# Optimization experiments

Measured on AMD Instinct MI355X. Metric: run time of the kernel, lower is better.

## Reference

```python
import jax, jax.numpy as jnp
import numpy as np

B, L, S, H, E, M = 16, 2048, 2048, 8, 64, 64  # batch, q len, kv len, heads, per-head dim, modes
SCALE = 1.0 / (512 * 512)  # 1/(in_channels*out_channels)


def setup_inputs() -> dict:
    key = jax.random.key(0)
    kq, kk, kv, kw1, kw2 = jax.random.split(key, 5)
    return {
        "q": jax.random.normal(kq, (B, L, H, E), dtype=jnp.float32),
        "k": jax.random.normal(kk, (B, S, H, E), dtype=jnp.float32),
        "v": jax.random.normal(kv, (B, S, H, E), dtype=jnp.float32),
        "weights_real": SCALE * jax.random.uniform(kw1, (H, E, E, M), dtype=jnp.float32),
        "weights_imag": SCALE * jax.random.uniform(kw2, (H, E, E, M), dtype=jnp.float32),
        "mask": jnp.zeros((1,), dtype=bool),  # unused by forward (kept for signature parity)
    }


def reference(q, k, v, weights_real, weights_imag, mask):
    # [B, L, H, E] -> [B, H, E, L]
    _q = jnp.transpose(q, (0, 2, 3, 1))
    _k = jnp.transpose(k, (0, 2, 3, 1))
    _v = jnp.transpose(v, (0, 2, 3, 1))

    # rFFT along time; mode_select_method='else' => index = range(M), a contiguous slice
    Qf = jnp.fft.rfft(_q, axis=-1)[..., :M]  # [B, H, E, M] complex
    Kf = jnp.fft.rfft(_k, axis=-1)[..., :M]
    Vf = jnp.fft.rfft(_v, axis=-1)[..., :M]

    # cross attention in frequency domain
    QK = jnp.einsum('bhex,bhey->bhxy', Qf, Kf)  # [B, H, M, M] complex
    QK = jnp.tanh(QK.real) + 1j * jnp.tanh(QK.imag)  # 'tanh' activation on re/im
    QKV = jnp.einsum('bhxy,bhey->bhex', QK, Vf)  # [B, H, E, M]

    W = (weights_real + 1j * weights_imag).astype(jnp.complex64)  # [H, E, O, M]
    QKVW = jnp.einsum('bhex,heox->bhox', QKV, W)  # [B, H, O, M]

    # scatter selected modes back into full half-spectrum, then inverse FFT
    Y = jnp.zeros((B, H, E, L // 2 + 1), dtype=jnp.complex64).at[..., :M].set(QKVW)
    y = jnp.fft.irfft(Y, n=L, axis=-1)  # [B, H, O, L] real
    return jnp.transpose(y, (0, 3, 1, 2))  # [B, L, H, O]
```

## Files before the change

### kernel.cpp

```cpp
#include <hip/hip_runtime.h>
#include <hip/hip_fp16.h>
#include <math.h>


#define NB 16
#define NL 2048
#define NH 8
#define NE 64
#define NM 64
#define NHE 512

typedef unsigned short ushort_t;
typedef __attribute__((ext_vector_type(8))) short short8;
typedef __attribute__((ext_vector_type(8))) _Float16 half8;
typedef __attribute__((ext_vector_type(4))) float f32x4;

__device__ inline void gld_lds16(const void* g, void* l) {
    __builtin_amdgcn_global_load_lds((const __attribute__((address_space(1))) unsigned int*)g,
                                     (__attribute__((address_space(3))) unsigned int*)l, 16, 0, 0);
}

__global__ __launch_bounds__(256) void k_tables_gemm(ushort_t* __restrict__ Twh,
                                                     ushort_t* __restrict__ Twl) {
    int i = blockIdx.x * 256 + threadIdx.x;
    int kj = i & 7;
    int l  = (i >> 3) & 63;
    int g  = (i >> 9) & 7;
    int ks = i >> 12;
    int mp = g * 16 + (l & 15);
    int kk = (l >> 4) * 8 + kj;
    int t = ks * 32 + kk;
    int m = mp >> 1;
    float ang = (float)((6.283185307179586476925287 / (double)NL) * (double)((m * t) & (NL - 1)));
    float val = (mp & 1) ? -sinf(ang) : cosf(ang);
    unsigned cb = __float_as_uint(val);
    ushort_t h = (ushort_t)(cb >> 16);
    float lo = val - __uint_as_float(cb & 0xffff0000u);
    unsigned lb = __float_as_uint(lo);
    unsigned r = lb + 0x7fffu + ((lb >> 16) & 1u);
    Twh[i] = h;
    Twl[i] = (ushort_t)(r >> 16);
}

__global__ __launch_bounds__(256) void k_tables_idft(ushort_t* __restrict__ Ih) {
    int i = blockIdx.x * 256 + threadIdx.x;
    int j = i & 7;
    int l = (i >> 3) & 63;
    int f = (i >> 9) & 15;
    int ks = (i >> 13) & 3;
    int tt = i >> 15;
    int t = tt * 256 + f * 16 + (l & 15);
    int kk = ks * 32 + (l >> 4) * 8 + j;
    int x = kk >> 1;
    float ang = (float)((6.283185307179586476925287 / (double)NL) * (double)((t * x) & (NL - 1)));
    float val = (kk & 1) ? -sinf(ang) : cosf(ang);
    Ih[i] = __half_as_ushort(__float2half(val));
}

__global__ __launch_bounds__(256, 3) void k_gemm(
    const float* __restrict__ q, const float* __restrict__ k, const float* __restrict__ v,
    const ushort_t* __restrict__ Twh, const ushort_t* __restrict__ Twl,
    float* __restrict__ Part) {
    const int bx = blockIdx.x & 3;
    const int kq = blockIdx.x >> 2;
    const int b  = blockIdx.y;
    const int z  = blockIdx.z;
    const float* __restrict__ in = (z == 0) ? q : ((z == 1) ? k : v);

    const int tid  = threadIdx.x;
    const int wid  = tid >> 6;
    const int lane = tid & 63;
    const int lr   = lane & 15;
    const int lg   = lane >> 4;

    __shared__ ushort_t Bh[2][4096];
    __shared__ ushort_t Bl[2][4096];

    f32x4 acc[2][8];
#pragma unroll
    for (int f = 0; f < 2; ++f)
#pragma unroll
        for (int g = 0; g < 8; ++g) acc[f][g] = (f32x4){0.f, 0.f, 0.f, 0.f};

    const float* pA = in + ((size_t)b * NL + (size_t)kq * 1024) * NHE + bx * 128 + wid * 32 + lr;

    float arE[2][8], arO[2][8];

#define STAGE_B(n, ksn)                                                               \
    {                                                                                 \
        const ushort_t* gh = Twh + (size_t)(kq * 32 + (ksn)) * 4096;                  \
        const ushort_t* gl = Twl + (size_t)(kq * 32 + (ksn)) * 4096;                  \
        gld_lds16(gh + (size_t)tid * 8, &Bh[n][tid * 8]);                             \
        gld_lds16(gh + (size_t)(tid + 256) * 8, &Bh[n][(tid + 256) * 8]);             \
        gld_lds16(gl + (size_t)tid * 8, &Bl[n][tid * 8]);                             \
        gld_lds16(gl + (size_t)(tid + 256) * 8, &Bl[n][(tid + 256) * 8]);             \
    }

#define LOADA(ar, ksn)                                                                \
    {                                                                                 \
        _Pragma("unroll")                                                             \
        for (int f = 0; f < 2; ++f) {                                                 \
            _Pragma("unroll")                                                         \
            for (int j = 0; j < 8; ++j)                                               \
                ar[f][j] = pA[(size_t)((ksn) * 32 + lg * 8 + j) * NHE + f * 16];      \
        }                                                                             \
    }

#define COMPUTE(ar, n)                                                                \
    {                                                                                 \
        short8 ah[2], al[2];                                                          \
        _Pragma("unroll")                                                             \
        for (int f = 0; f < 2; ++f) {                                                 \
            union { unsigned u[4]; short8 s; } uh, ul;                                \
            _Pragma("unroll")                                                         \
            for (int p = 0; p < 4; ++p) {                                             \
                unsigned b0 = __float_as_uint(ar[f][2 * p]);                          \
                unsigned b1 = __float_as_uint(ar[f][2 * p + 1]);                      \
                uh.u[p] = (b0 >> 16) | (b1 & 0xffff0000u);                            \
                float l0 = ar[f][2 * p]     - __uint_as_float(b0 & 0xffff0000u);      \
                float l1 = ar[f][2 * p + 1] - __uint_as_float(b1 & 0xffff0000u);      \
                unsigned lw;                                                          \
                asm("v_cvt_pk_bf16_f32 %0, %1, %2" : "=v"(lw) : "v"(l0), "v"(l1));    \
                ul.u[p] = lw;                                                         \
            }                                                                         \
            ah[f] = uh.s; al[f] = ul.s;                                               \
        }                                                                             \
        _Pragma("unroll")                                                             \
        for (int g = 0; g < 8; ++g) {                                                 \
            short8 bh8 = *(const short8*)&Bh[n][(g * 64 + lane) * 8];                 \
            short8 bl8 = *(const short8*)&Bl[n][(g * 64 + lane) * 8];                 \
            _Pragma("unroll")                                                         \
            for (int f = 0; f < 2; ++f) {                                             \
                acc[f][g] = __builtin_amdgcn_mfma_f32_16x16x32_bf16(ah[f], bh8, acc[f][g], 0, 0, 0); \
                acc[f][g] = __builtin_amdgcn_mfma_f32_16x16x32_bf16(al[f], bh8, acc[f][g], 0, 0, 0); \
                acc[f][g] = __builtin_amdgcn_mfma_f32_16x16x32_bf16(ah[f], bl8, acc[f][g], 0, 0, 0); \
            }                                                                         \
        }                                                                             \
    }

    STAGE_B(0, 0);
    LOADA(arE, 0);

#pragma unroll 1
    for (int k2 = 0; k2 < 16; ++k2) {
        const int ksB = 2 * k2 + 1;
        __syncthreads();
        STAGE_B(1, ksB);
        LOADA(arO, ksB);
        COMPUTE(arE, 0);
        __syncthreads();
        if (k2 < 15) {
            STAGE_B(0, ksB + 1);
            LOADA(arE, ksB + 1);
        }
        COMPUTE(arO, 1);
    }
#undef STAGE_B
#undef LOADA
#undef COMPUTE

    float* pout = Part + (size_t)(z * 2 + kq) * 1048576;
#pragma unroll
    for (int f = 0; f < 2; ++f) {
#pragma unroll
        for (int g = 0; g < 8; ++g) {
            const int col = g * 16 + lr;
#pragma unroll
            for (int r = 0; r < 4; ++r) {
                const int he = bx * 128 + wid * 32 + f * 16 + 4 * lg + r;
                pout[((size_t)b * NHE + he) * 128 + col] = acc[f][g][r];
            }
        }
    }
}

__global__ __launch_bounds__(256) void k_reduce(
    const float4* __restrict__ Part, float4* __restrict__ Qf,
    float4* __restrict__ Kf, float4* __restrict__ Vf) {
    int i = blockIdx.x * 256 + threadIdx.x;
    int z = i >> 18;
    int r = i & 262143;
    float4 a = Part[(size_t)(z * 2 + 0) * 262144 + r];
    float4 b = Part[(size_t)(z * 2 + 1) * 262144 + r];
    float4 s = make_float4(a.x + b.x, a.y + b.y, a.z + b.z, a.w + b.w);
    float4* o = (z == 0) ? Qf : ((z == 1) ? Kf : Vf);
    o[r] = s;
}

__global__ __launch_bounds__(256) void k_qk(
    const float2* __restrict__ Qf, const float2* __restrict__ Kf,
    float2* __restrict__ QKt) {
    const int bh = blockIdx.x;
    const int xh = blockIdx.y;
    const int tid = threadIdx.x;
    __shared__ float2 Qs[64 * 34];
    __shared__ float2 Ks[64 * 66];

    const float2* Qbase = Qf + (size_t)bh * (NE * NM);
    const float2* Kbase = Kf + (size_t)bh * (NE * NM);
#pragma unroll
    for (int j = 0; j < 4; ++j) {
        int n = tid + j * 256;
        int e = n >> 4, c = n & 15;
        float4 val = ((const float4*)(Qbase + e * NM + xh * 32))[c];
        *((float4*)&Qs[e * 34 + c * 2]) = val;
    }
#pragma unroll
    for (int j = 0; j < 8; ++j) {
        int n = tid + j * 256;
        int e = n >> 5, c = n & 31;
        float4 val = ((const float4*)(Kbase + e * NM))[c];
        *((float4*)&Ks[e * 66 + c * 2]) = val;
    }
    __syncthreads();

    const int yq = tid & 31, xq = tid >> 5;
    float accr[4][2], acci[4][2];
#pragma unroll
    for (int i = 0; i < 4; ++i)
#pragma unroll
        for (int j = 0; j < 2; ++j) { accr[i][j] = 0.f; acci[i][j] = 0.f; }

    for (int e = 0; e < 64; ++e) {
        float4 qa = *((float4*)&Qs[e * 34 + xq * 4]);
        float4 qb = *((float4*)&Qs[e * 34 + xq * 4 + 2]);
        float4 kk = *((float4*)&Ks[e * 66 + yq * 2]);
        float qr[4] = {qa.x, qa.z, qb.x, qb.z};
        float qi[4] = {qa.y, qa.w, qb.y, qb.w};
        float kr[2] = {kk.x, kk.z};
        float ki[2] = {kk.y, kk.w};
#pragma unroll
        for (int i = 0; i < 4; ++i) {
#pragma unroll
            for (int j = 0; j < 2; ++j) {
                accr[i][j] += qr[i] * kr[j] - qi[i] * ki[j];
                acci[i][j] += qr[i] * ki[j] + qi[i] * kr[j];
            }
        }
    }
    const int x0 = xh * 32 + xq * 4;
#pragma unroll
    for (int i = 0; i < 4; ++i) {
        float4 sv = make_float4(tanhf(accr[i][0]), tanhf(acci[i][0]),
                                tanhf(accr[i][1]), tanhf(acci[i][1]));
        *((float4*)&QKt[(size_t)bh * 4096 + (x0 + i) * 64 + yq * 2]) = sv;
    }
}

__global__ __launch_bounds__(256) void k_qkv(
    const float2* __restrict__ Vf, const float2* __restrict__ QKt,
    float2* __restrict__ QKV) {
    const int bh = blockIdx.x;
    const int eh = blockIdx.y;
    const int tid = threadIdx.x;
    __shared__ float2 Vs[32 * 66];
    __shared__ float2 Ps[64 * 66];

    const float2* Vbase = Vf + (size_t)bh * (NE * NM) + eh * 32 * NM;
    const float2* Pbase = QKt + (size_t)bh * 4096;
#pragma unroll
    for (int j = 0; j < 4; ++j) {
        int n = tid + j * 256;
        int r = n >> 5, c = n & 31;
        float4 val = ((const float4*)(Vbase + r * NM))[c];
        *((float4*)&Vs[r * 66 + c * 2]) = val;
    }
#pragma unroll
    for (int j = 0; j < 8; ++j) {
        int n = tid + j * 256;
        int r = n >> 5, c = n & 31;
        float4 val = ((const float4*)(Pbase + r * NM))[c];
        *((float4*)&Ps[r * 66 + c * 2]) = val;
    }
    __syncthreads();

    const int xq = tid & 15, eq2 = tid >> 4;
    const int x0 = xq * 4, e0 = eq2 * 2;
    float accr[2][4], acci[2][4];
#pragma unroll
    for (int i = 0; i < 2; ++i)
#pragma unroll
        for (int j = 0; j < 4; ++j) { accr[i][j] = 0.f; acci[i][j] = 0.f; }

    for (int yy = 0; yy < 64; ++yy) {
        float2 v0 = Vs[(e0 + 0) * 66 + yy];
        float2 v1 = Vs[(e0 + 1) * 66 + yy];
        float2 p0 = Ps[(x0 + 0) * 66 + yy];
        float2 p1 = Ps[(x0 + 1) * 66 + yy];
        float2 p2 = Ps[(x0 + 2) * 66 + yy];
        float2 p3 = Ps[(x0 + 3) * 66 + yy];
        float pr[4] = {p0.x, p1.x, p2.x, p3.x};
        float pi[4] = {p0.y, p1.y, p2.y, p3.y};
#pragma unroll
        for (int j = 0; j < 4; ++j) {
            accr[0][j] += v0.x * pr[j] - v0.y * pi[j];
            acci[0][j] += v0.x * pi[j] + v0.y * pr[j];
            accr[1][j] += v1.x * pr[j] - v1.y * pi[j];
            acci[1][j] += v1.x * pi[j] + v1.y * pr[j];
        }
    }
#pragma unroll
    for (int e = 0; e < 2; ++e) {
        float2* obase = QKV + (size_t)bh * 4096 + (eh * 32 + e0 + e) * 64 + x0;
        float4 s0 = make_float4(accr[e][0], acci[e][0], accr[e][1], acci[e][1]);
        float4 s1 = make_float4(accr[e][2], acci[e][2], accr[e][3], acci[e][3]);
        ((float4*)obase)[0] = s0;
        ((float4*)obase)[1] = s1;
    }
}

__global__ __launch_bounds__(256) void k_wt(
    const float* __restrict__ wr, const float* __restrict__ wi,
    float2* __restrict__ Wt) {
    const int e = blockIdx.x, h = blockIdx.y;
    const int tid = threadIdx.x;
    __shared__ float lr[64 * 68];
    __shared__ float li[64 * 68];
    const float* rbase = wr + (size_t)(h * NE + e) * NE * NM;
    const float* ibase = wi + (size_t)(h * NE + e) * NE * NM;
#pragma unroll
    for (int j = 0; j < 4; ++j) {
        int n = tid + j * 256;
        int o = n >> 4, x4 = n & 15;
        float4 r4 = ((const float4*)(rbase + o * NM))[x4];
        float4 i4 = ((const float4*)(ibase + o * NM))[x4];
        *((float4*)&lr[o * 68 + x4 * 4]) = r4;
        *((float4*)&li[o * 68 + x4 * 4]) = i4;
    }
    __syncthreads();
#pragma unroll
    for (int j = 0; j < 16; ++j) {
        int n = tid + j * 256;
        int x = n >> 6, o = n & 63;
        Wt[((size_t)(h * NM + x) * NE + e) * NE + o] =
            make_float2(lr[o * 68 + x], li[o * 68 + x]);
    }
}

__global__ __launch_bounds__(256) void k_qkvw(
    const float2* __restrict__ QKV, const float2* __restrict__ Wt,
    float2* __restrict__ QKVWs) {
    const int x = blockIdx.x, h = blockIdx.y;
    const int tid = threadIdx.x;
    const int o = tid & 63, bq = tid >> 6;
    float accr[4], acci[4];
#pragma unroll
    for (int j = 0; j < 4; ++j) { accr[j] = 0.f; acci[j] = 0.f; }

    const float2* wbase = Wt + (size_t)(h * NM + x) * NE * NE + o;
    for (int e = 0; e < 64; ++e) {
        float2 w = wbase[(size_t)e * NE];
#pragma unroll
        for (int j = 0; j < 4; ++j) {
            int b = bq * 4 + j;
            float2 a = QKV[((size_t)(b * NH + h) * NE + e) * NM + x];
            accr[j] += a.x * w.x - a.y * w.y;
            acci[j] += a.x * w.y + a.y * w.x;
        }
    }
    const float sc = (x == 0) ? 0.5f : 1.0f;
#pragma unroll
    for (int j = 0; j < 4; ++j) {
        int b = bq * 4 + j;
        QKVWs[((size_t)(b * NH + h) * NM + x) * NE + o] =
            make_float2(accr[j] * sc, acci[j] * sc);
    }
}

__global__ __launch_bounds__(256, 3) void k_idft(
    const float2* __restrict__ QKVWs, const ushort_t* __restrict__ Ih,
    float* __restrict__ yout) {
    const int tt = blockIdx.x;
    const int bh = blockIdx.y;
    const int b = bh >> 3, h = bh & 7;
    const int tid = threadIdx.x;
    const int wid = tid >> 6;
    const int lane = tid & 63;
    const int lr = lane & 15;
    const int lg = lane >> 4;

    __shared__ ushort_t Ta[8192];
    __shared__ unsigned Xs[4096];

    const float2* xb = QKVWs + (size_t)bh * 4096;
#pragma unroll
    for (int r = 0; r < 16; ++r) {
        int i = tid + r * 256;
        int x = i >> 6, o = i & 63;
        float2 val = xb[i];
        int ks = x >> 4;
        int lane2 = (((x & 15) >> 2) << 4) | (o & 15);
        int jn = o >> 4;
        unsigned pk = (unsigned)__half_as_ushort(__float2half(val.x)) |
                      ((unsigned)__half_as_ushort(__float2half(val.y)) << 16);
        Xs[((ks * 4 + jn) * 64 + lane2) * 4 + (x & 3)] = pk;
    }
    {
        const ushort_t* gh = Ih + (size_t)(tt * 4) * 8192;
#pragma unroll
        for (int p = 0; p < 4; ++p)
            gld_lds16(gh + (size_t)(tid + p * 256) * 8, &Ta[(tid + p * 256) * 8]);
    }
    __syncthreads();

    f32x4 acc[4][4];
#pragma unroll
    for (int m = 0; m < 4; ++m)
#pragma unroll
        for (int n = 0; n < 4; ++n) acc[m][n] = (f32x4){0.f, 0.f, 0.f, 0.f};

    const ushort_t* XsS = (const ushort_t*)Xs;
    for (int ks = 0; ks < 4; ++ks) {
        half8 ah[4], bx_[4];
#pragma unroll
        for (int m = 0; m < 4; ++m)
            ah[m] = *(const half8*)&Ta[((wid * 4 + m) * 64 + lane) * 8];
#pragma unroll
        for (int n = 0; n < 4; ++n)
            bx_[n] = *(const half8*)&XsS[((ks * 4 + n) * 64 + lane) * 8];
#pragma unroll
        for (int m = 0; m < 4; ++m)
#pragma unroll
            for (int n = 0; n < 4; ++n)
                acc[m][n] = __builtin_amdgcn_mfma_f32_16x16x32_f16(ah[m], bx_[n], acc[m][n], 0, 0, 0);
        if (ks < 3) {
            __syncthreads();
            const ushort_t* gh = Ih + (size_t)(tt * 4 + ks + 1) * 8192;
#pragma unroll
            for (int p = 0; p < 4; ++p)
                gld_lds16(gh + (size_t)(tid + p * 256) * 8, &Ta[(tid + p * 256) * 8]);
            __syncthreads();
        }
    }

    const int t0 = tt * 256 + wid * 64;
    const float inv = 1.f / 1024.f;
#pragma unroll
    for (int m = 0; m < 4; ++m) {
#pragma unroll
        for (int n = 0; n < 4; ++n) {
            const int o = n * 16 + lr;
#pragma unroll
            for (int r = 0; r < 4; ++r) {
                const int t = t0 + m * 16 + lg * 4 + r;
                yout[(((size_t)b * NL + t) * NH + h) * NE + o] = acc[m][n][r] * inv;
            }
        }
    }
}

extern "C" void kernel_launch(void* const* d_in, const int* in_sizes, int n_in,
                              void* d_out, int out_size, void* d_ws, size_t ws_size,
                              hipStream_t stream) {
    const float* q  = (const float*)d_in[0];
    const float* k  = (const float*)d_in[1];
    const float* v  = (const float*)d_in[2];
    const float* wr = (const float*)d_in[3];
    const float* wi = (const float*)d_in[4];
    float* out = (float*)d_out;

    char* w = (char*)d_ws;
    ushort_t* Twh  = (ushort_t*)w;
    ushort_t* Twl  = (ushort_t*)(w + 524288);
    ushort_t* Ih   = (ushort_t*)(w + 1048576);
    float2*   Qf   = (float2*)(w + 2097152);
    float2*   Kf   = (float2*)(w + 6291456);
    float2*   Vf   = (float2*)(w + 10485760);
    float*    Part = (float*)(w + 14680064);
    float2*   QKt  = (float2*)(w + 14680064);
    float2*   QKV  = (float2*)(w + 18874368);
    float2*   Wt   = (float2*)(w + 23068672);
    float2*   QKVWs= (float2*)(w + 39845888);

    hipLaunchKernelGGL(k_tables_gemm, dim3(1024), dim3(256), 0, stream, Twh, Twl);
    hipLaunchKernelGGL(k_tables_idft, dim3(1024), dim3(256), 0, stream, Ih);
    hipLaunchKernelGGL(k_gemm, dim3(8, 16, 3), dim3(256), 0, stream,
                       q, k, v, Twh, Twl, Part);
    hipLaunchKernelGGL(k_reduce, dim3(3072), dim3(256), 0, stream,
                       (const float4*)Part, (float4*)Qf, (float4*)Kf, (float4*)Vf);
    hipLaunchKernelGGL(k_qk, dim3(128, 2), dim3(256), 0, stream, Qf, Kf, QKt);
    hipLaunchKernelGGL(k_qkv, dim3(128, 2), dim3(256), 0, stream, Vf, QKt, QKV);
    hipLaunchKernelGGL(k_wt, dim3(64, 8), dim3(256), 0, stream, wr, wi, Wt);
    hipLaunchKernelGGL(k_qkvw, dim3(64, 8), dim3(256), 0, stream, QKV, Wt, QKVWs);
    hipLaunchKernelGGL(k_idft, dim3(8, 128), dim3(256), 0, stream, QKVWs, Ih, out);
}
```

Before: 150.9 us.

## Drop LDS staging in DFT GEMM; load twiddle tiles directly from global per wave

Removes the shared-memory double buffer and barriers for the twiddle (B) operand. Each wave now reads its B fragments straight from global memory (relying on L1/L2 caching), and the two K-halves are split across waves within a block instead of across blocks. This cuts __syncthreads overhead and LDS traffic. In exchange it raises register pressure from holding 16 short8 B fragments, drops the occupancy hint in launch bounds, and multiplies global/L2 reads of the twiddle table. The grid launch is presumably changed elsewhere to match the new block indexing.

```diff
diff --git a/kernel.cpp b/kernel.cpp
--- a/kernel.cpp
+++ b/kernel.cpp
@@ -57,12 +57,11 @@
     Ih[i] = __half_as_ushort(__float2half(val));
 }
 
-__global__ __launch_bounds__(256, 3) void k_gemm(
+__global__ __launch_bounds__(256) void k_gemm(
     const float* __restrict__ q, const float* __restrict__ k, const float* __restrict__ v,
     const ushort_t* __restrict__ Twh, const ushort_t* __restrict__ Twl,
     float* __restrict__ Part) {
-    const int bx = blockIdx.x & 3;
-    const int kq = blockIdx.x >> 2;
+    const int bx = blockIdx.x;
     const int b  = blockIdx.y;
     const int z  = blockIdx.z;
     const float* __restrict__ in = (z == 0) ? q : ((z == 1) ? k : v);
@@ -72,9 +71,8 @@
     const int lane = tid & 63;
     const int lr   = lane & 15;
     const int lg   = lane >> 4;
-
-    __shared__ ushort_t Bh[2][4096];
-    __shared__ ushort_t Bl[2][4096];
+    const int hc   = bx * 2 + (wid >> 1);
+    const int kq   = wid & 1;
 
     f32x4 acc[2][8];
 #pragma unroll
@@ -82,32 +80,32 @@
 #pragma unroll
         for (int g = 0; g < 8; ++g) acc[f][g] = (f32x4){0.f, 0.f, 0.f, 0.f};
 
-    const float* pA = in + ((size_t)b * NL + (size_t)kq * 1024) * NHE + bx * 128 + wid * 32 + lr;
+    const float* pA = in + ((size_t)b * NL + (size_t)kq * 1024) * NHE + hc * 32 + lr;
+    const ushort_t* pBh = Twh + (size_t)kq * 32 * 4096 + lane * 8;
+    const ushort_t* pBl = Twl + (size_t)kq * 32 * 4096 + lane * 8;
 
     float arE[2][8], arO[2][8];
-
-#define STAGE_B(n, ksn)                                                               \
-    {                                                                                 \
-        const ushort_t* gh = Twh + (size_t)(kq * 32 + (ksn)) * 4096;                  \
-        const ushort_t* gl = Twl + (size_t)(kq * 32 + (ksn)) * 4096;                  \
-        gld_lds16(gh + (size_t)tid * 8, &Bh[n][tid * 8]);                             \
-        gld_lds16(gh + (size_t)(tid + 256) * 8, &Bh[n][(tid + 256) * 8]);             \
-        gld_lds16(gl + (size_t)tid * 8, &Bl[n][tid * 8]);                             \
-        gld_lds16(gl + (size_t)(tid + 256) * 8, &Bl[n][(tid + 256) * 8]);             \
-    }
 
 #define LOADA(ar, ksn)                                                                \
     {                                                                                 \
         _Pragma("unroll")                                                             \
         for (int f = 0; f < 2; ++f) {                                                 \
             _Pragma("unroll")                                                         \
-            for (int j = 0; j < 8; ++j)                                               \
-                ar[f][j] = pA[(size_t)((ksn) * 32 + lg * 8 + j) * NHE + f * 16];      \
+            for (int jj = 0; jj < 8; ++jj)                                            \
+                ar[f][jj] = pA[(size_t)((ksn) * 32 + lg * 8 + jj) * NHE + f * 16];    \
         }                                                                             \
     }
 
-#define COMPUTE(ar, n)                                                                \
+#define COMPUTE(ar, ksn)                                                              \
     {                                                                                 \
+        const ushort_t* bhp = pBh + (size_t)(ksn) * 4096;                             \
+        const ushort_t* blp = pBl + (size_t)(ksn) * 4096;                             \
+        short8 bh8[8], bl8[8];                                                        \
+        _Pragma("unroll")                                                             \
+        for (int j = 0; j < 8; ++j) {                                                 \
+            bh8[j] = *(const short8*)(bhp + j * 512);                                 \
+            bl8[j] = *(const short8*)(blp + j * 512);                                 \
+        }                                                                             \
         short8 ah[2], al[2];                                                          \
         _Pragma("unroll")                                                             \
         for (int f = 0; f < 2; ++f) {                                                 \
@@ -126,36 +124,25 @@
             ah[f] = uh.s; al[f] = ul.s;                                               \
         }                                                                             \
         _Pragma("unroll")                                                             \
-        for (int g = 0; g < 8; ++g) {                                                 \
-            short8 bh8 = *(const short8*)&Bh[n][(g * 64 + lane) * 8];                 \
-            short8 bl8 = *(const short8*)&Bl[n][(g * 64 + lane) * 8];                 \
+        for (int j = 0; j < 8; ++j) {                                                 \
             _Pragma("unroll")                                                         \
             for (int f = 0; f < 2; ++f) {                                             \
-                acc[f][g] = __builtin_amdgcn_mfma_f32_16x16x32_bf16(ah[f], bh8, acc[f][g], 0, 0, 0); \
-                acc[f][g] = __builtin_amdgcn_mfma_f32_16x16x32_bf16(al[f], bh8, acc[f][g], 0, 0, 0); \
-                acc[f][g] = __builtin_amdgcn_mfma_f32_16x16x32_bf16(ah[f], bl8, acc[f][g], 0, 0, 0); \
+                acc[f][j] = __builtin_amdgcn_mfma_f32_16x16x32_bf16(ah[f], bh8[j], acc[f][j], 0, 0, 0); \
+                acc[f][j] = __builtin_amdgcn_mfma_f32_16x16x32_bf16(al[f], bh8[j], acc[f][j], 0, 0, 0); \
+                acc[f][j] = __builtin_amdgcn_mfma_f32_16x16x32_bf16(ah[f], bl8[j], acc[f][j], 0, 0, 0); \
             }                                                                         \
         }                                                                             \
     }
 
-    STAGE_B(0, 0);
     LOADA(arE, 0);
-
 #pragma unroll 1
     for (int k2 = 0; k2 < 16; ++k2) {
-        const int ksB = 2 * k2 + 1;
-        __syncthreads();
-        STAGE_B(1, ksB);
-        LOADA(arO, ksB);
-        COMPUTE(arE, 0);
-        __syncthreads();
-        if (k2 < 15) {
-            STAGE_B(0, ksB + 1);
-            LOADA(arE, ksB + 1);
-        }
-        COMPUTE(arO, 1);
-    }
-#undef STAGE_B
+        const int ksO = 2 * k2 + 1;
+        LOADA(arO, ksO);
+        COMPUTE(arE, 2 * k2);
+        if (k2 < 15) LOADA(arE, ksO + 1);
+        COMPUTE(arO, ksO);
+    }
 #undef LOADA
 #undef COMPUTE
 
@@ -163,12 +150,12 @@
 #pragma unroll
     for (int f = 0; f < 2; ++f) {
 #pragma unroll
-        for (int g = 0; g < 8; ++g) {
-            const int col = g * 16 + lr;
+        for (int j = 0; j < 8; ++j) {
+            const int col = j * 16 + lr;
 #pragma unroll
             for (int r = 0; r < 4; ++r) {
-                const int he = bx * 128 + wid * 32 + f * 16 + 4 * lg + r;
-                pout[((size_t)b * NHE + he) * 128 + col] = acc[f][g][r];
+                const int he = hc * 32 + f * 16 + 4 * lg + r;
+                pout[((size_t)b * NHE + he) * 128 + col] = acc[f][j][r];
             }
         }
     }
```

Measured after the change: 182.6 us. 21.1% more time.
